# Performance work log

Measured on AMD Instinct MI355X. Metric: run time of the kernel, lower is better.

The kernel has to match this reference:

```python
import jax, jax.numpy as jnp
import numpy as np

N_NODES = 50000
N_EDGES = 800000
D_IN = 128
D_HID = 128
D_OUT = 128


def setup_inputs() -> dict:
    key = jax.random.key(0)
    ks = jax.random.split(key, 6)
    x = jax.random.normal(ks[0], (N_NODES, D_IN), dtype=jnp.float32)
    edge_index = jax.random.randint(ks[1], (2, N_EDGES), 0, N_NODES, dtype=jnp.int64)
    s_in = 1.0 / np.sqrt(D_IN)
    s_hid = 1.0 / np.sqrt(D_HID)
    W1 = jax.random.normal(ks[2], (D_IN, D_HID), dtype=jnp.float32) * s_in
    b1 = jnp.zeros((D_HID,), dtype=jnp.float32)
    W2 = jax.random.normal(ks[3], (D_HID, D_OUT), dtype=jnp.float32) * s_hid
    b2 = jnp.zeros((D_OUT,), dtype=jnp.float32)
    return {"x": x, "edge_index": edge_index, "W1": W1, "b1": b1, "W2": W2, "b2": b2}


def gcn_conv(x, src, dst, W, b):
    # x: [N, Din]; src/dst: [E+N] (self-loops already appended)
    N = x.shape[0]
    h = x @ W  # [N, Dout] dense transform first (PyG GCNConv order)
    deg = jnp.zeros((N,), h.dtype).at[dst].add(jnp.ones((), h.dtype))
    dinv = jax.lax.rsqrt(deg)  # deg >= 1 thanks to self-loops
    norm = dinv[src] * dinv[dst]  # [E+N] symmetric normalization
    msg = h[src] * norm[:, None]  # per-edge gathered messages
    out = jax.ops.segment_sum(msg, dst, num_segments=N)
    return out + b


def reference(x, edge_index, W1, b1, W2, b2):
    N = x.shape[0]
    loop = jnp.arange(N, dtype=edge_index.dtype)
    src = jnp.concatenate([edge_index[0], loop])
    dst = jnp.concatenate([edge_index[1], loop])
    h = jax.nn.relu(gcn_conv(x, src, dst, W1, b1))
    out = gcn_conv(h, src, dst, W2, b2)
    return out
```

## Files before the change

### kernel.cpp

```cpp
#include <hip/hip_runtime.h>

#define N_NODES 50000
#define N_EDGES 800000
#define D 128
#define NBUK 196
#define HB 128
#define EPB 6250

typedef __attribute__((ext_vector_type(8))) short bf16x8;
typedef __attribute__((ext_vector_type(4))) float f32x4;

__device__ inline unsigned short f2bf(float f) {
    unsigned u = __float_as_uint(f);
    u += 0x7fffu + ((u >> 16) & 1u);
    return (unsigned short)(u >> 16);
}
__device__ inline float bf2f(unsigned short h) {
    return __uint_as_float((unsigned)h << 16);
}

__global__ __launch_bounds__(256) void prep_hist_kernel(const float* __restrict__ W1,
                                                        const float* __restrict__ W2,
                                                        unsigned short* __restrict__ Wt,
                                                        const int* __restrict__ dst,
                                                        int* __restrict__ H) {
    __shared__ int hist[NBUK];
    const int b = blockIdx.x;
    const int t = threadIdx.x;
    if (b < 128) {
        int tid = b * 256 + t;
        int a = tid >> 14;
        int idx = tid & 16383;
        const float* W = a ? W2 : W1;
        float w = W[idx];
        unsigned short hi = f2bf(w);
        unsigned short lo = f2bf(w - bf2f(hi));
        int k = idx >> 7, col = idx & 127;
        int byte = (col * 128 + k) * 2;
        int swz = byte ^ (((byte >> 8) & 7) << 4);
        unsigned short* base = Wt + a * 32768;
        *(unsigned short*)((char*)base + swz) = hi;
        *(unsigned short*)((char*)(base + 16384) + swz) = lo;
    } else {
        const int blk = b - 128;
        if (t < NBUK) hist[t] = 0;
        __syncthreads();
        const int e0 = blk * EPB;
        for (int i = t; i < EPB; i += 256)
            atomicAdd(&hist[dst[e0 + i] >> 8], 1);
        __syncthreads();
        if (t < NBUK) H[blk * NBUK + t] = hist[t];
    }
}

__global__ __launch_bounds__(256) void kscan_kernel(const int* __restrict__ H,
                                                    int* __restrict__ B,
                                                    int* __restrict__ bbase,
                                                    int* __restrict__ bsize) {
    __shared__ int s[256];
    const int t = threadIdx.x;
    int sum = 0;
    if (t < NBUK)
        for (int blk = 0; blk < HB; ++blk) sum += H[blk * NBUK + t];
    s[t] = sum;
    __syncthreads();
    #pragma unroll
    for (int off = 1; off < 256; off <<= 1) {
        int add = (t >= off) ? s[t - off] : 0;
        __syncthreads();
        s[t] += add;
        __syncthreads();
    }
    int base = s[t] - sum;
    if (t < NBUK) {
        bbase[t] = base;
        bsize[t] = sum;
        int run = base;
        for (int blk = 0; blk < HB; ++blk) {
            B[blk * NBUK + t] = run;
            run += H[blk * NBUK + t];
        }
    }
}

__global__ __launch_bounds__(256) void kstage_kernel(const int* __restrict__ src,
                                                     const int* __restrict__ dst,
                                                     const int* __restrict__ B,
                                                     unsigned* __restrict__ stage) {
    __shared__ int cur[NBUK];
    const int t = threadIdx.x;
    if (t < NBUK) cur[t] = B[blockIdx.x * NBUK + t];
    __syncthreads();
    const int e0 = blockIdx.x * EPB;
    for (int i = t; i < EPB; i += 256) {
        int d = dst[e0 + i];
        int s = src[e0 + i];
        int pos = atomicAdd(&cur[d >> 8], 1);
        stage[pos] = (unsigned)s | ((unsigned)(d & 255) << 16);
    }
}

__global__ __launch_bounds__(256) void gemm1_final_kernel(
        const float* __restrict__ A, const unsigned short* __restrict__ Wt,
        unsigned short* __restrict__ Cb, int M, int ngemm,
        const unsigned* __restrict__ stage, const int* __restrict__ bbase,
        const int* __restrict__ bsize, int* __restrict__ cnt, int* __restrict__ offs,
        float* __restrict__ dinv, int* __restrict__ csr) {
    __shared__ char smem[65536];
    const int tid = threadIdx.x;

    if ((int)blockIdx.x < ngemm) {
        unsigned short* lds = (unsigned short*)smem;
        #pragma unroll
        for (int i = 0; i < 16; ++i) {
            int off = i * 4096 + tid * 16;
            *(uint4*)((char*)lds + off) = *(const uint4*)((const char*)Wt + off);
        }
        const int lane = tid & 63;
        const int wave = tid >> 6;
        const int c = lane & 15;
        const int g = lane >> 4;
        const int arow_i = blockIdx.x * 64 + wave * 16 + c;
        const bool inb = arow_i < M;
        const float* arow = A + (size_t)arow_i * D;

        bf16x8 ah[4], al[4];
        #pragma unroll
        for (int s = 0; s < 4; ++s) {
            int k0 = s * 32 + g * 8;
            float4 v0 = {0.f, 0.f, 0.f, 0.f}, v1 = {0.f, 0.f, 0.f, 0.f};
            if (inb) {
                v0 = *(const float4*)(arow + k0);
                v1 = *(const float4*)(arow + k0 + 4);
            }
            float av[8] = {v0.x, v0.y, v0.z, v0.w, v1.x, v1.y, v1.z, v1.w};
            #pragma unroll
            for (int j = 0; j < 8; ++j) {
                float f = av[j];
                unsigned short h = f2bf(f);
                unsigned short l = f2bf(f - bf2f(h));
                ah[s][j] = (short)h;
                al[s][j] = (short)l;
            }
        }
        __syncthreads();

        f32x4 acc[8];
        #pragma unroll
        for (int t = 0; t < 8; ++t) { f32x4 z = {0.f, 0.f, 0.f, 0.f}; acc[t] = z; }

        const int xmask = (lane & 7) << 4;
        #pragma unroll
        for (int s = 0; s < 4; ++s) {
            int lowk = (s * 64 + g * 16) ^ xmask;
            #pragma unroll
            for (int t = 0; t < 8; ++t) {
                int off = t * 4096 + c * 256 + lowk;
                bf16x8 bh = *(const bf16x8*)((const char*)lds + off);
                bf16x8 bl = *(const bf16x8*)((const char*)lds + 32768 + off);
                acc[t] = __builtin_amdgcn_mfma_f32_16x16x32_bf16(al[s], bh, acc[t], 0, 0, 0);
                acc[t] = __builtin_amdgcn_mfma_f32_16x16x32_bf16(ah[s], bl, acc[t], 0, 0, 0);
                acc[t] = __builtin_amdgcn_mfma_f32_16x16x32_bf16(ah[s], bh, acc[t], 0, 0, 0);
            }
        }

        const int r0 = blockIdx.x * 64 + wave * 16 + g * 4;
        #pragma unroll
        for (int t = 0; t < 8; ++t) {
            #pragma unroll
            for (int r = 0; r < 4; ++r) {
                int grow = r0 + r;
                if (grow < M) Cb[(size_t)grow * D + t * 16 + c] = f2bf(acc[t][r]);
            }
        }
    } else {
        int* hist = (int*)smem;
        int* s    = hist + 256;
        const int t = tid;
        const int k = blockIdx.x - ngemm;
        const int base = bbase[k];
        const int size = bsize[k];
        hist[t] = 0;
        __syncthreads();
        for (int i = t; i < size; i += 256)
            atomicAdd(&hist[stage[base + i] >> 16], 1);
        __syncthreads();
        int deg = hist[t];
        s[t] = deg;
        __syncthreads();
        #pragma unroll
        for (int off = 1; off < 256; off <<= 1) {
            int add = (t >= off) ? s[t - off] : 0;
            __syncthreads();
            s[t] += add;
            __syncthreads();
        }
        int excl = s[t] - deg;
        int node = k * 256 + t;
        if (node < N_NODES) {
            cnt[node] = deg;
            offs[node] = base + excl;
            dinv[node] = rsqrtf((float)deg + 1.0f);
        }
        hist[t] = base + excl;
        __syncthreads();
        for (int i = t; i < size; i += 256) {
            unsigned v = stage[base + i];
            int pos = atomicAdd(&hist[v >> 16], 1);
            csr[pos] = (int)(v & 0xffffu);
        }
    }
}

__global__ __launch_bounds__(256) void mfma_gemm_relu_kernel(const float* __restrict__ A,
                                                             const unsigned short* __restrict__ Wt,
                                                             unsigned short* __restrict__ Cb,
                                                             int M) {
    __shared__ unsigned short lds[32768];
    const int tid = threadIdx.x;
    #pragma unroll
    for (int i = 0; i < 16; ++i) {
        int off = i * 4096 + tid * 16;
        *(uint4*)((char*)lds + off) = *(const uint4*)((const char*)Wt + off);
    }
    const int lane = tid & 63;
    const int wave = tid >> 6;
    const int c = lane & 15;
    const int g = lane >> 4;
    const int arow_i = blockIdx.x * 64 + wave * 16 + c;
    const bool inb = arow_i < M;
    const float* arow = A + (size_t)arow_i * D;

    bf16x8 ah[4], al[4];
    #pragma unroll
    for (int s = 0; s < 4; ++s) {
        int k0 = s * 32 + g * 8;
        float4 v0 = {0.f, 0.f, 0.f, 0.f}, v1 = {0.f, 0.f, 0.f, 0.f};
        if (inb) {
            v0 = *(const float4*)(arow + k0);
            v1 = *(const float4*)(arow + k0 + 4);
        }
        float av[8] = {v0.x, v0.y, v0.z, v0.w, v1.x, v1.y, v1.z, v1.w};
        #pragma unroll
        for (int j = 0; j < 8; ++j) {
            float f = fmaxf(av[j], 0.f);
            unsigned short h = f2bf(f);
            unsigned short l = f2bf(f - bf2f(h));
            ah[s][j] = (short)h;
            al[s][j] = (short)l;
        }
    }
    __syncthreads();

    f32x4 acc[8];
    #pragma unroll
    for (int t = 0; t < 8; ++t) { f32x4 z = {0.f, 0.f, 0.f, 0.f}; acc[t] = z; }

    const int xmask = (lane & 7) << 4;
    #pragma unroll
    for (int s = 0; s < 4; ++s) {
        int lowk = (s * 64 + g * 16) ^ xmask;
        #pragma unroll
        for (int t = 0; t < 8; ++t) {
            int off = t * 4096 + c * 256 + lowk;
            bf16x8 bh = *(const bf16x8*)((const char*)lds + off);
            bf16x8 bl = *(const bf16x8*)((const char*)lds + 32768 + off);
            acc[t] = __builtin_amdgcn_mfma_f32_16x16x32_bf16(al[s], bh, acc[t], 0, 0, 0);
            acc[t] = __builtin_amdgcn_mfma_f32_16x16x32_bf16(ah[s], bl, acc[t], 0, 0, 0);
            acc[t] = __builtin_amdgcn_mfma_f32_16x16x32_bf16(ah[s], bh, acc[t], 0, 0, 0);
        }
    }

    const int r0 = blockIdx.x * 64 + wave * 16 + g * 4;
    #pragma unroll
    for (int t = 0; t < 8; ++t) {
        #pragma unroll
        for (int r = 0; r < 4; ++r) {
            int grow = r0 + r;
            if (grow < M) Cb[(size_t)grow * D + t * 16 + c] = f2bf(acc[t][r]);
        }
    }
}

__global__ __launch_bounds__(256) void gather_kernel(const unsigned short* __restrict__ hnb,
                                                     const float* __restrict__ dinv,
                                                     const int* __restrict__ offs,
                                                     const int* __restrict__ cnt,
                                                     const int* __restrict__ csr,
                                                     const float* __restrict__ bias,
                                                     float* __restrict__ out) {
    const int wid = threadIdx.x >> 6;
    const int lane = threadIdx.x & 63;
    const int n = blockIdx.x * 4 + wid;
    if (n >= N_NODES) return;
    const int beg = offs[n];
    const int m = cnt[n];
    const int col = lane * 2;

    float ax = 0.f, ay = 0.f;
    int i = 0;
    for (; i + 8 <= m; i += 8) {
        int sidx[8];
        #pragma unroll
        for (int j = 0; j < 8; ++j) sidx[j] = csr[beg + i + j];
        float w[8];
        unsigned v[8];
        #pragma unroll
        for (int j = 0; j < 8; ++j) {
            w[j] = dinv[sidx[j]];
            v[j] = *(const unsigned*)(hnb + (size_t)sidx[j] * D + col);
        }
        #pragma unroll
        for (int j = 0; j < 8; ++j) {
            ax = fmaf(w[j], __uint_as_float(v[j] << 16), ax);
            ay = fmaf(w[j], __uint_as_float(v[j] & 0xffff0000u), ay);
        }
    }
    for (; i + 4 <= m; i += 4) {
        int sidx[4];
        #pragma unroll
        for (int j = 0; j < 4; ++j) sidx[j] = csr[beg + i + j];
        #pragma unroll
        for (int j = 0; j < 4; ++j) {
            float w = dinv[sidx[j]];
            unsigned v = *(const unsigned*)(hnb + (size_t)sidx[j] * D + col);
            ax = fmaf(w, __uint_as_float(v << 16), ax);
            ay = fmaf(w, __uint_as_float(v & 0xffff0000u), ay);
        }
    }
    for (; i < m; ++i) {
        int s = csr[beg + i];
        float w = dinv[s];
        unsigned v = *(const unsigned*)(hnb + (size_t)s * D + col);
        ax = fmaf(w, __uint_as_float(v << 16), ax);
        ay = fmaf(w, __uint_as_float(v & 0xffff0000u), ay);
    }
    float dn = dinv[n];
    float dn2 = dn * dn;
    unsigned hv = *(const unsigned*)(hnb + (size_t)n * D + col);
    float2 bv = *(const float2*)&bias[col];
    float ox = fmaf(dn, ax, fmaf(dn2, __uint_as_float(hv << 16), bv.x));
    float oy = fmaf(dn, ay, fmaf(dn2, __uint_as_float(hv & 0xffff0000u), bv.y));
    float2 o = {ox, oy};
    *(float2*)&out[(size_t)n * D + col] = o;
}

extern "C" void kernel_launch(void* const* d_in, const int* in_sizes, int n_in,
                              void* d_out, int out_size, void* d_ws, size_t ws_size,
                              hipStream_t stream) {
    const float* x  = (const float*)d_in[0];
    const int*   ei = (const int*)d_in[1];
    const float* W1 = (const float*)d_in[2];
    const float* b1 = (const float*)d_in[3];
    const float* W2 = (const float*)d_in[4];
    const float* b2 = (const float*)d_in[5];
    float* out = (float*)d_out;

    const int* src = ei;
    const int* dst = ei + N_EDGES;

    int* wsi = (int*)d_ws;
    int*      cnt   = wsi;
    int*      offs  = cnt + 50176;
    float*    dinv  = (float*)(offs + 50176);
    int*      bbase = (int*)(dinv + 50176);
    int*      bsize = bbase + 256;
    int*      H     = bsize + 256;
    int*      B     = H + 25088;
    unsigned* stage = (unsigned*)(B + 25088);
    int*      csr   = (int*)(stage + 800000);
    unsigned short* Wt = (unsigned short*)(csr + 800000);
    unsigned short* hn = Wt + 65536;
    float* agg1 = (float*)(hn + (size_t)N_NODES * D + 64);

    const int Bt = 256;
    const int gemm_grid = (N_NODES + 63) / 64;
    const int gather_grid = (N_NODES + 3) / 4;

    prep_hist_kernel<<<256, Bt, 0, stream>>>(W1, W2, Wt, dst, H);
    kscan_kernel<<<1, Bt, 0, stream>>>(H, B, bbase, bsize);
    kstage_kernel<<<HB, Bt, 0, stream>>>(src, dst, B, stage);

    gemm1_final_kernel<<<gemm_grid + NBUK, Bt, 0, stream>>>(
        x, Wt, hn, N_NODES, gemm_grid,
        stage, bbase, bsize, cnt, offs, dinv, csr);

    gather_kernel<<<gather_grid, Bt, 0, stream>>>(hn, dinv, offs, cnt, csr, b1, agg1);

    mfma_gemm_relu_kernel<<<gemm_grid, Bt, 0, stream>>>(agg1, Wt + 32768, hn, N_NODES);
    gather_kernel<<<gather_grid, Bt, 0, stream>>>(hn, dinv, offs, cnt, csr, b2, out);
}
```

Before: 212.5 us.

## Fuse layer-1 gather with GEMM2 and fold bucket scan into consumers

```diff
diff --git a/kernel.cpp b/kernel.cpp
--- a/kernel.cpp
+++ b/kernel.cpp
@@ -53,45 +53,34 @@
     }
 }
 
-__global__ __launch_bounds__(256) void kscan_kernel(const int* __restrict__ H,
-                                                    int* __restrict__ B,
-                                                    int* __restrict__ bbase,
-                                                    int* __restrict__ bsize) {
-    __shared__ int s[256];
+__global__ __launch_bounds__(256) void kstage_kernel(const int* __restrict__ src,
+                                                     const int* __restrict__ dst,
+                                                     const int* __restrict__ H,
+                                                     unsigned* __restrict__ stage) {
+    __shared__ int cur[256];
+    __shared__ int sarr[256];
     const int t = threadIdx.x;
-    int sum = 0;
-    if (t < NBUK)
-        for (int blk = 0; blk < HB; ++blk) sum += H[blk * NBUK + t];
-    s[t] = sum;
+    const int myb = blockIdx.x;
+    int tot = 0, pre = 0;
+    if (t < NBUK) {
+        for (int b = 0; b < HB; ++b) {
+            int h = H[b * NBUK + t];
+            tot += h;
+            if (b < myb) pre += h;
+        }
+    }
+    sarr[t] = (t < NBUK) ? tot : 0;
     __syncthreads();
     #pragma unroll
     for (int off = 1; off < 256; off <<= 1) {
-        int add = (t >= off) ? s[t - off] : 0;
-        __syncthreads();
-        s[t] += add;
-        __syncthreads();
-    }
-    int base = s[t] - sum;
-    if (t < NBUK) {
-        bbase[t] = base;
-        bsize[t] = sum;
-        int run = base;
-        for (int blk = 0; blk < HB; ++blk) {
-            B[blk * NBUK + t] = run;
-            run += H[blk * NBUK + t];
-        }
-    }
-}
-
-__global__ __launch_bounds__(256) void kstage_kernel(const int* __restrict__ src,
-                                                     const int* __restrict__ dst,
-                                                     const int* __restrict__ B,
-                                                     unsigned* __restrict__ stage) {
-    __shared__ int cur[NBUK];
-    const int t = threadIdx.x;
-    if (t < NBUK) cur[t] = B[blockIdx.x * NBUK + t];
+        int add = (t >= off) ? sarr[t - off] : 0;
+        __syncthreads();
+        sarr[t] += add;
+        __syncthreads();
+    }
+    if (t < NBUK) cur[t] = (sarr[t] - tot) + pre;
     __syncthreads();
-    const int e0 = blockIdx.x * EPB;
+    const int e0 = myb * EPB;
     for (int i = t; i < EPB; i += 256) {
         int d = dst[e0 + i];
         int s = src[e0 + i];
@@ -103,8 +92,8 @@
 __global__ __launch_bounds__(256) void gemm1_final_kernel(
         const float* __restrict__ A, const unsigned short* __restrict__ Wt,
         unsigned short* __restrict__ Cb, int M, int ngemm,
-        const unsigned* __restrict__ stage, const int* __restrict__ bbase,
-        const int* __restrict__ bsize, int* __restrict__ cnt, int* __restrict__ offs,
+        const unsigned* __restrict__ stage, const int* __restrict__ H,
+        int* __restrict__ cnt, int* __restrict__ offs,
         float* __restrict__ dinv, int* __restrict__ csr) {
     __shared__ char smem[65536];
     const int tid = threadIdx.x;
@@ -175,27 +164,43 @@
         }
     } else {
         int* hist = (int*)smem;
-        int* s    = hist + 256;
+        int* sarr = hist + 256;
+        int* csum = sarr + 256;
         const int t = tid;
         const int k = blockIdx.x - ngemm;
-        const int base = bbase[k];
-        const int size = bsize[k];
+        int tot = 0;
+        if (t < NBUK)
+            for (int b = 0; b < HB; ++b) tot += H[b * NBUK + t];
+        csum[t] = (t < NBUK) ? tot : 0;
+        sarr[t] = csum[t];
+        __syncthreads();
+        #pragma unroll
+        for (int off = 1; off < 256; off <<= 1) {
+            int add = (t >= off) ? sarr[t - off] : 0;
+            __syncthreads();
+            sarr[t] += add;
+            __syncthreads();
+        }
+        const int base = sarr[k] - csum[k];
+        const int size = csum[k];
+        __syncthreads();
+
         hist[t] = 0;
         __syncthreads();
         for (int i = t; i < size; i += 256)
             atomicAdd(&hist[stage[base + i] >> 16], 1);
         __syncthreads();
         int deg = hist[t];
-        s[t] = deg;
+        sarr[t] = deg;
         __syncthreads();
         #pragma unroll
         for (int off = 1; off < 256; off <<= 1) {
-            int add = (t >= off) ? s[t - off] : 0;
+            int add = (t >= off) ? sarr[t - off] : 0;
             __syncthreads();
-            s[t] += add;
+            sarr[t] += add;
             __syncthreads();
         }
-        int excl = s[t] - deg;
+        int excl = sarr[t] - deg;
         int node = k * 256 + t;
         if (node < N_NODES) {
             cnt[node] = deg;
@@ -212,45 +217,93 @@
     }
 }
 
-__global__ __launch_bounds__(256) void mfma_gemm_relu_kernel(const float* __restrict__ A,
-                                                             const unsigned short* __restrict__ Wt,
-                                                             unsigned short* __restrict__ Cb,
-                                                             int M) {
-    __shared__ unsigned short lds[32768];
+__global__ __launch_bounds__(256) void gather_gemm2_kernel(
+        const unsigned short* __restrict__ hnb, const float* __restrict__ dinv,
+        const int* __restrict__ offs, const int* __restrict__ cnt,
+        const int* __restrict__ csr, const float* __restrict__ bias1,
+        const unsigned short* __restrict__ Wt2, unsigned short* __restrict__ hn2) {
+    __shared__ float agg[64][132];
     const int tid = threadIdx.x;
-    #pragma unroll
-    for (int i = 0; i < 16; ++i) {
-        int off = i * 4096 + tid * 16;
-        *(uint4*)((char*)lds + off) = *(const uint4*)((const char*)Wt + off);
-    }
     const int lane = tid & 63;
     const int wave = tid >> 6;
+    const int col = lane * 2;
+    const float2 bv = *(const float2*)&bias1[col];
+
+    for (int nn = 0; nn < 16; ++nn) {
+        const int n = blockIdx.x * 64 + wave * 16 + nn;
+        float ox = 0.f, oy = 0.f;
+        if (n < N_NODES) {
+            const int beg = offs[n];
+            const int m = cnt[n];
+            float ax = 0.f, ay = 0.f;
+            int i = 0;
+            for (; i + 8 <= m; i += 8) {
+                int sidx[8];
+                #pragma unroll
+                for (int j = 0; j < 8; ++j) sidx[j] = csr[beg + i + j];
+                float w[8];
+                unsigned v[8];
+                #pragma unroll
+                for (int j = 0; j < 8; ++j) {
+                    w[j] = dinv[sidx[j]];
+                    v[j] = *(const unsigned*)(hnb + (size_t)sidx[j] * D + col);
+                }
+                #pragma unroll
+                for (int j = 0; j < 8; ++j) {
+                    ax = fmaf(w[j], __uint_as_float(v[j] << 16), ax);
+                    ay = fmaf(w[j], __uint_as_float(v[j] & 0xffff0000u), ay);
+                }
+            }
+            for (; i + 4 <= m; i += 4) {
+                int sidx[4];
+                #pragma unroll
+                for (int j = 0; j < 4; ++j) sidx[j] = csr[beg + i + j];
+                #pragma unroll
+                for (int j = 0; j < 4; ++j) {
+                    float w = dinv[sidx[j]];
+                    unsigned v = *(const unsigned*)(hnb + (size_t)sidx[j] * D + col);
+                    ax = fmaf(w, __uint_as_float(v << 16), ax);
+                    ay = fmaf(w, __uint_as_float(v & 0xffff0000u), ay);
+                }
+            }
+            for (; i < m; ++i) {
+                int s = csr[beg + i];
+                float w = dinv[s];
+                unsigned v = *(const unsigned*)(hnb + (size_t)s * D + col);
+                ax = fmaf(w, __uint_as_float(v << 16), ax);
+                ay = fmaf(w, __uint_as_float(v & 0xffff0000u), ay);
+            }
+            const float dn = dinv[n];
+            const float dn2 = dn * dn;
+            const unsigned hv = *(const unsigned*)(hnb + (size_t)n * D + col);
+            ox = fmaxf(fmaf(dn, ax, fmaf(dn2, __uint_as_float(hv << 16), bv.x)), 0.f);
+            oy = fmaxf(fmaf(dn, ay, fmaf(dn2, __uint_as_float(hv & 0xffff0000u), bv.y)), 0.f);
+        }
+        float2 o = {ox, oy};
+        *(float2*)&agg[wave * 16 + nn][col] = o;
+    }
+    __syncthreads();
+
     const int c = lane & 15;
     const int g = lane >> 4;
-    const int arow_i = blockIdx.x * 64 + wave * 16 + c;
-    const bool inb = arow_i < M;
-    const float* arow = A + (size_t)arow_i * D;
+    const int arow = wave * 16 + c;
 
     bf16x8 ah[4], al[4];
     #pragma unroll
     for (int s = 0; s < 4; ++s) {
         int k0 = s * 32 + g * 8;
-        float4 v0 = {0.f, 0.f, 0.f, 0.f}, v1 = {0.f, 0.f, 0.f, 0.f};
-        if (inb) {
-            v0 = *(const float4*)(arow + k0);
-            v1 = *(const float4*)(arow + k0 + 4);
-        }
+        float4 v0 = *(const float4*)&agg[arow][k0];
+        float4 v1 = *(const float4*)&agg[arow][k0 + 4];
         float av[8] = {v0.x, v0.y, v0.z, v0.w, v1.x, v1.y, v1.z, v1.w};
         #pragma unroll
         for (int j = 0; j < 8; ++j) {
-            float f = fmaxf(av[j], 0.f);
+            float f = av[j];
             unsigned short h = f2bf(f);
             unsigned short l = f2bf(f - bf2f(h));
             ah[s][j] = (short)h;
             al[s][j] = (short)l;
         }
     }
-    __syncthreads();
 
     f32x4 acc[8];
     #pragma unroll
@@ -263,8 +316,8 @@
         #pragma unroll
         for (int t = 0; t < 8; ++t) {
             int off = t * 4096 + c * 256 + lowk;
-            bf16x8 bh = *(const bf16x8*)((const char*)lds + off);
-            bf16x8 bl = *(const bf16x8*)((const char*)lds + 32768 + off);
+            bf16x8 bh = *(const bf16x8*)((const char*)Wt2 + off);
+            bf16x8 bl = *(const bf16x8*)((const char*)Wt2 + 32768 + off);
             acc[t] = __builtin_amdgcn_mfma_f32_16x16x32_bf16(al[s], bh, acc[t], 0, 0, 0);
             acc[t] = __builtin_amdgcn_mfma_f32_16x16x32_bf16(ah[s], bl, acc[t], 0, 0, 0);
             acc[t] = __builtin_amdgcn_mfma_f32_16x16x32_bf16(ah[s], bh, acc[t], 0, 0, 0);
@@ -277,7 +330,7 @@
         #pragma unroll
         for (int r = 0; r < 4; ++r) {
             int grow = r0 + r;
-            if (grow < M) Cb[(size_t)grow * D + t * 16 + c] = f2bf(acc[t][r]);
+            if (grow < N_NODES) hn2[(size_t)grow * D + t * 16 + c] = f2bf(acc[t][r]);
         }
     }
 }
@@ -363,30 +416,26 @@
     int*      cnt   = wsi;
     int*      offs  = cnt + 50176;
     float*    dinv  = (float*)(offs + 50176);
-    int*      bbase = (int*)(dinv + 50176);
-    int*      bsize = bbase + 256;
-    int*      H     = bsize + 256;
-    int*      B     = H + 25088;
-    unsigned* stage = (unsigned*)(B + 25088);
+    int*      H     = (int*)(dinv + 50176);
+    unsigned* stage = (unsigned*)(H + 25088);
     int*      csr   = (int*)(stage + 800000);
-    unsigned short* Wt = (unsigned short*)(csr + 800000);
-    unsigned short* hn = Wt + 65536;
-    float* agg1 = (float*)(hn + (size_t)N_NODES * D + 64);
+    unsigned short* Wt  = (unsigned short*)(csr + 800000);
+    unsigned short* hn  = Wt + 65536;
+    unsigned short* hn2 = hn + (size_t)N_NODES * D + 64;
 
     const int Bt = 256;
     const int gemm_grid = (N_NODES + 63) / 64;
     const int gather_grid = (N_NODES + 3) / 4;
 
     prep_hist_kernel<<<256, Bt, 0, stream>>>(W1, W2, Wt, dst, H);
-    kscan_kernel<<<1, Bt, 0, stream>>>(H, B, bbase, bsize);
-    kstage_kernel<<<HB, Bt, 0, stream>>>(src, dst, B, stage);
+    kstage_kernel<<<HB, Bt, 0, stream>>>(src, dst, H, stage);
 
     gemm1_final_kernel<<<gemm_grid + NBUK, Bt, 0, stream>>>(
         x, Wt, hn, N_NODES, gemm_grid,
-        stage, bbase, bsize, cnt, offs, dinv, csr);
-
-    gather_kernel<<<gather_grid, Bt, 0, stream>>>(hn, dinv, offs, cnt, csr, b1, agg1);
-
-    mfma_gemm_relu_kernel<<<gemm_grid, Bt, 0, stream>>>(agg1, Wt + 32768, hn, N_NODES);
-    gather_kernel<<<gather_grid, Bt, 0, stream>>>(hn, dinv, offs, cnt, csr, b2, out);
-}
+        stage, H, cnt, offs, dinv, csr);
+
+    gather_gemm2_kernel<<<gemm_grid, Bt, 0, stream>>>(
+        hn, dinv, offs, cnt, csr, b1, Wt + 32768, hn2);
+
+    gather_kernel<<<gather_grid, Bt, 0, stream>>>(hn2, dinv, offs, cnt, csr, b2, out);
+}
```

Result: slower. 229.1 us (+7.8%).
